# Kernel optimization log

Hardware: AMD Instinct MI355X
Metric: run time of the kernel (lower is better)

Reference implementation:

```python
import jax, jax.numpy as jnp
import numpy as np

IGNORE = 5
N_CLASS = 5
MAX_VIEWS = 2048
MAX_VIEWS_BG = 4096


def setup_inputs() -> dict:
    key = jax.random.key(0)
    ks = jax.random.split(key, 8)
    B, C, H, W = 8, 512, 128, 128
    HF, WF = 1024, 1024
    feats = jax.random.normal(ks[0], (B, C, H, W), dtype=jnp.float32)
    labels = jax.random.uniform(ks[1], (B, HF, WF, N_CLASS), dtype=jnp.float32)
    predicts = jax.random.randint(ks[2], (B, H, W), 0, N_CLASS).astype(jnp.int32)
    s = 0.02
    w1 = jax.random.normal(ks[3], (512, 512), jnp.float32) * s
    b1 = jnp.zeros((512,), jnp.float32)
    w2 = jax.random.normal(ks[4], (256, 512), jnp.float32) * s
    b2 = jnp.zeros((256,), jnp.float32)
    w3 = jax.random.normal(ks[5], (256, 256), jnp.float32) * s
    b3 = jnp.zeros((256,), jnp.float32)
    return dict(feats=feats, labels=labels, predicts=predicts,
                w1=w1, b1=b1, w2=w2, b2=b2, w3=w3, b3=b3)


def _leaky(x):
    return jnp.where(x >= 0, x, 0.2 * x)


def _proj_head(x, w1, b1, w2, b2, w3, b3):
    # Linear -> LeakyReLU(0.2) -> Linear -> LeakyReLU(0.2) -> Linear, then L2-normalize (dim=1)
    h = _leaky(x @ w1.T + b1)
    h = _leaky(h @ w2.T + b2)
    h = h @ w3.T + b3
    nrm = jnp.maximum(jnp.linalg.norm(h, axis=1, keepdims=True), 1e-12)
    return h / nrm


def _sample_class(y_hat, y, feats0, c, mv):
    """Stratified hard/easy pixel selection for class c, padded to static size mv.
    Deterministic take-first-k replaces torch.randperm for reproducibility."""
    N = y_hat.shape[0]
    hard = (y_hat == c) & (y != c)
    easy = (y_hat == c) & (y == c)
    nh = hard.sum().astype(jnp.int32)
    ne = easy.sum().astype(jnp.int32)
    cnt = nh + ne
    valid = (cnt > 1).astype(jnp.int32)   # classes with <=1 pixel are skipped in the original
    n_sel = jnp.minimum(cnt, mv) * valid
    both = (2 * nh >= n_sel) & (2 * ne >= n_sel)
    hk = jnp.where(both, n_sel // 2,
                   jnp.where(2 * nh >= n_sel, n_sel - ne, nh))
    ek = n_sel - hk
    idx = jnp.arange(N, dtype=jnp.int32)
    hsel = hard & ((jnp.cumsum(hard) - 1) < hk)   # first hk hard pixels
    esel = easy & ((jnp.cumsum(easy) - 1) < ek)   # first ek easy pixels
    # stream-compaction: hard first, then easy, then padding
    sort_key = jnp.where(hsel, idx, jnp.where(esel, idx + N, 2 * N))
    order = jnp.argsort(sort_key)[:mv]            # static slice of size mv
    row_ok = jnp.arange(mv) < n_sel
    X = feats0[order] * row_ok[:, None]           # zero-pad invalid rows
    yc = jnp.where(row_ok, c, IGNORE)
    return X, yc.astype(jnp.int32)


def reference(feats, labels, predicts, w1, b1, w2, b2, w3, b3):
    B, C, H, W = feats.shape
    lab = jnp.argmax(labels, axis=-1)             # [B, HF, WF]
    sh, sw = lab.shape[1] // H, lab.shape[2] // W
    lab_ds = lab[:, ::sh, ::sw]                   # nearest-neighbor downsample (integer factor)
    # original _hard_anchor_sampling returns inside the batch loop -> only image 0 contributes
    y_hat = lab_ds[0].reshape(-1).astype(jnp.int32)
    y = predicts[0].reshape(-1).astype(jnp.int32)
    feats0 = feats[0].transpose(1, 2, 0).reshape(H * W, C)  # NHWC flatten
    Xs, ys = [], []
    for c in range(N_CLASS):                      # static small class loop
        mv = MAX_VIEWS_BG if c == 0 else MAX_VIEWS
        Xc, yc = _sample_class(y_hat, y, feats0, c, mv)
        Xs.append(Xc)
        ys.append(yc)
    X_ = jnp.concatenate(Xs, axis=0)              # [MV_bg + 4*MV, 512]
    y_ = jnp.concatenate(ys, axis=0)
    anchors = _proj_head(X_, w1, b1, w2, b2, w3, b3)
    return anchors, y_
```

## Files before the change

kernel.cpp:

```cpp
#include <hip/hip_runtime.h>

#define HW 16384
#define IGN 5
#define ROWS_TOTAL 12288
#define ANCH_ELEMS (ROWS_TOTAL * 256)

typedef __bf16 bf16x8 __attribute__((ext_vector_type(8)));
typedef float f32x4 __attribute__((ext_vector_type(4)));
typedef unsigned long long ull;

#define GLDS16(g, l)                                                                     \
    __builtin_amdgcn_global_load_lds((__attribute__((address_space(1))) const void*)(g), \
                                     (__attribute__((address_space(3))) void*)(l), 16, 0, 0)

__device__ __forceinline__ int swz_off(int row, int chunk) {
    return row * 64 + ((chunk ^ (row & 7)) * 8);
}

__global__ void prep_fused(const float* __restrict__ labels, const int* __restrict__ predicts,
                           int* __restrict__ y_hat, ull* __restrict__ maskH,
                           ull* __restrict__ maskE, int* __restrict__ fwd,
                           const float* __restrict__ w1, const float* __restrict__ w2,
                           const float* __restrict__ w3, __bf16* __restrict__ w1b,
                           __bf16* __restrict__ w2b, __bf16* __restrict__ w3b,
                           const float* __restrict__ F, __bf16* __restrict__ Xb) {
    __shared__ float t[64][68];
    int bid = blockIdx.x;
    int tid = threadIdx.x;
    if (bid < 64) {
        int p = bid * 256 + tid;
        int pr = p >> 7, pc = p & 127;
        const float* lp = labels + ((size_t)(pr * 8) * 1024 + (size_t)(pc * 8)) * 5;
        float best = lp[0];
        int bi = 0;
#pragma unroll
        for (int c = 1; c < 5; ++c) {
            float v = lp[c];
            if (v > best) { best = v; bi = c; }
        }
        y_hat[p] = bi;
        if (p < ROWS_TOTAL) fwd[p] = -1;
        int yy = predicts[p];
        int chunk = p >> 6;
        int lane = tid & 63;
#pragma unroll
        for (int c = 0; c < 5; ++c) {
            ull mh = __ballot(bi == c && yy != c);
            ull me = __ballot(bi == c && yy == c);
            if (lane == 0) {
                maskH[c * 256 + chunk] = mh;
                maskE[c * 256 + chunk] = me;
            }
        }
    } else if (bid < 512) {
        int base = ((bid - 64) * 256 + tid) * 4;
        if (base < 262144) {
            float4 v = *(const float4*)(w1 + base);
            w1b[base + 0] = (__bf16)v.x; w1b[base + 1] = (__bf16)v.y;
            w1b[base + 2] = (__bf16)v.z; w1b[base + 3] = (__bf16)v.w;
        } else if (base < 393216) {
            int o = base - 262144;
            float4 v = *(const float4*)(w2 + o);
            w2b[o + 0] = (__bf16)v.x; w2b[o + 1] = (__bf16)v.y;
            w2b[o + 2] = (__bf16)v.z; w2b[o + 3] = (__bf16)v.w;
        } else {
            int o = base - 393216;
            float4 v = *(const float4*)(w3 + o);
            w3b[o + 0] = (__bf16)v.x; w3b[o + 1] = (__bf16)v.y;
            w3b[o + 2] = (__bf16)v.z; w3b[o + 3] = (__bf16)v.w;
        }
    } else {
        int cid = bid - 512;
        int pb = (cid & 255) * 64;
        int chb = (cid >> 8) * 64;
        int row = tid >> 2;
        int seg = tid & 3;
        const float* src = F + (size_t)(chb + row) * HW + pb + seg * 16;
#pragma unroll
        for (int k = 0; k < 4; ++k)
            *(float4*)&t[row][seg * 16 + k * 4] = *(const float4*)(src + k * 4);
        __syncthreads();
        int p = tid >> 2;
        __bf16* dst = Xb + (size_t)(pb + p) * 512 + chb + seg * 16;
        bf16x8 o0, o1;
#pragma unroll
        for (int j = 0; j < 8; ++j) o0[j] = (__bf16)t[seg * 16 + j][p];
#pragma unroll
        for (int j = 0; j < 8; ++j) o1[j] = (__bf16)t[seg * 16 + 8 + j][p];
        *(bf16x8*)dst = o0;
        *(bf16x8*)(dst + 8) = o1;
    }
}

__global__ void scan_kernel(const ull* __restrict__ maskH, const ull* __restrict__ maskE,
                            int* __restrict__ baseH, int* __restrict__ baseE,
                            int* __restrict__ nsel, int* __restrict__ hkA,
                            int* __restrict__ ekA) {
    int c = threadIdx.x >> 6;
    int lane = threadIdx.x & 63;
    if (c >= 5) return;
    int ph[4], pe[4];
    int sh = 0, se = 0;
#pragma unroll
    for (int k = 0; k < 4; ++k) {
        int ch = lane * 4 + k;
        ph[k] = sh;
        sh += __popcll(maskH[c * 256 + ch]);
        pe[k] = se;
        se += __popcll(maskE[c * 256 + ch]);
    }
    int incH = sh, incE = se;
#pragma unroll
    for (int d = 1; d < 64; d <<= 1) {
        int t = __shfl_up(incH, d);
        if (lane >= d) incH += t;
        t = __shfl_up(incE, d);
        if (lane >= d) incE += t;
    }
    int exH = incH - sh, exE = incE - se;
#pragma unroll
    for (int k = 0; k < 4; ++k) {
        baseH[c * 256 + lane * 4 + k] = exH + ph[k];
        baseE[c * 256 + lane * 4 + k] = exE + pe[k];
    }
    int nh = __shfl(incH, 63), ne = __shfl(incE, 63);
    if (lane == 0) {
        int mv = (c == 0) ? 4096 : 2048;
        int cnt = nh + ne;
        int n_sel = (cnt > 1) ? ((cnt < mv) ? cnt : mv) : 0;
        int hk;
        if ((2 * nh >= n_sel) && (2 * ne >= n_sel)) hk = n_sel >> 1;
        else if (2 * nh >= n_sel) hk = n_sel - ne;
        else hk = nh;
        nsel[c] = n_sel;
        hkA[c] = hk;
        ekA[c] = n_sel - hk;
    }
}

__global__ void write_inv_kernel(const int* __restrict__ y_hat,
                                 const ull* __restrict__ maskH, const ull* __restrict__ maskE,
                                 const int* __restrict__ baseH, const int* __restrict__ baseE,
                                 const int* __restrict__ hkA, const int* __restrict__ ekA,
                                 const int* __restrict__ nsel, int* __restrict__ fwd,
                                 float* __restrict__ out) {
    int p = blockIdx.x * 256 + threadIdx.x;
    int chunk = p >> 6;
    int lane = threadIdx.x & 63;
    int c = y_hat[p];
    ull mh = maskH[c * 256 + chunk];
    ull me = maskE[c * 256 + chunk];
    ull below = (1ull << lane) - 1ull;
    int cls_base = (c == 0) ? 0 : 4096 + (c - 1) * 2048;
    int res = -1;
    if ((mh >> lane) & 1ull) {
        int pos = baseH[c * 256 + chunk] + __popcll(mh & below);
        if (pos < hkA[c]) res = cls_base + pos;
    } else if ((me >> lane) & 1ull) {
        int pos = baseE[c * 256 + chunk] + __popcll(me & below);
        if (pos < ekA[c]) res = cls_base + hkA[c] + pos;
    }
    if (res >= 0) fwd[res] = p;
    if (p < ROWS_TOTAL) {
        int cc, rin;
        if (p < 4096) { cc = 0; rin = p; }
        else { cc = 1 + ((p - 4096) >> 11); rin = (p - 4096) & 2047; }
        out[ANCH_ELEMS + p] = (float)(rin < nsel[cc] ? cc : IGN);
    }
}

__global__ __launch_bounds__(256) void gemm_bt(const __bf16* __restrict__ A,
                                               const int* __restrict__ fwd,
                                               const __bf16* __restrict__ Bw,
                                               const float* __restrict__ bias,
                                               __bf16* __restrict__ C, int N, int K,
                                               int leaky) {
    const int BK = 64;
    __shared__ __bf16 As[64 * 64];
    __shared__ __bf16 Bs[128 * 64];
    int tid = threadIdx.x;
    int lane = tid & 63;
    int wave_base = tid & 0xC0;
    int wave = tid >> 6;
    int wm = (wave >> 1) * 32, wn = (wave & 1) * 64;
    int mb = blockIdx.x * 64, nb = blockIdx.y * 128;
    int l15 = lane & 15, quad = lane >> 4;

    const __bf16* srcA[2];
    const __bf16* srcB[4];
#pragma unroll
    for (int r = 0; r < 2; ++r) {
        int cc = tid + r * 256;
        int row = cc >> 3, ch = cc & 7;
        int g = mb + row;
        int pix = fwd ? fwd[g] : g;
        if (pix < 0) pix = 0;
        srcA[r] = A + (size_t)pix * K + ((ch ^ (row & 7)) * 8);
    }
#pragma unroll
    for (int r = 0; r < 4; ++r) {
        int cc = tid + r * 256;
        int row = cc >> 3, ch = cc & 7;
        srcB[r] = Bw + (size_t)(nb + row) * K + ((ch ^ (row & 7)) * 8);
    }

    f32x4 acc[2][4] = {};

    for (int kt = 0; kt < K; kt += BK) {
#pragma unroll
        for (int r = 0; r < 2; ++r)
            GLDS16(srcA[r] + kt, As + (size_t)(r * 256 + wave_base) * 8);
#pragma unroll
        for (int r = 0; r < 4; ++r)
            GLDS16(srcB[r] + kt, Bs + (size_t)(r * 256 + wave_base) * 8);
        __syncthreads();
#pragma unroll
        for (int kk = 0; kk < 2; ++kk) {
            bf16x8 af[2], bq[4];
#pragma unroll
            for (int i = 0; i < 2; ++i)
                af[i] = *(const bf16x8*)(As + swz_off(wm + i * 16 + l15, quad + kk * 4));
#pragma unroll
            for (int j = 0; j < 4; ++j)
                bq[j] = *(const bf16x8*)(Bs + swz_off(wn + j * 16 + l15, quad + kk * 4));
#pragma unroll
            for (int i = 0; i < 2; ++i)
#pragma unroll
                for (int j = 0; j < 4; ++j)
                    acc[i][j] = __builtin_amdgcn_mfma_f32_16x16x32_bf16(af[i], bq[j], acc[i][j], 0, 0, 0);
        }
        __syncthreads();
    }

#pragma unroll
    for (int i = 0; i < 2; ++i) {
#pragma unroll
        for (int j = 0; j < 4; ++j) {
            int col = nb + wn + j * 16 + l15;
            float bv = bias[col];
#pragma unroll
            for (int r = 0; r < 4; ++r) {
                int row = mb + wm + i * 16 + quad * 4 + r;
                float v = acc[i][j][r] + bv;
                if (leaky) v = (v >= 0.f) ? v : 0.2f * v;
                C[(size_t)row * N + col] = (__bf16)v;
            }
        }
    }
}

__global__ __launch_bounds__(256) void gemm23_norm(const __bf16* __restrict__ H1,
                                                   const __bf16* __restrict__ W2b,
                                                   const float* __restrict__ b2,
                                                   const __bf16* __restrict__ W3b,
                                                   const float* __restrict__ b3,
                                                   const int* __restrict__ fwd,
                                                   float* __restrict__ out) {
    __shared__ __bf16 As[32 * 64];
    __shared__ __bf16 Ws[256 * 64];
    __shared__ __bf16 H2s[4][32 * 64];
    __shared__ float nrm[32];
    int tid = threadIdx.x;
    int lane = tid & 63, wave = tid >> 6;
    int wave_base = tid & 0xC0;
    int l15 = lane & 15, quad = lane >> 4;
    int mb = blockIdx.x * 32;
    int wn = wave * 64;

    if (tid < 32) nrm[tid] = 0.f;

    int rowA = tid >> 3, chA = tid & 7;
    const __bf16* srcA = H1 + (size_t)(mb + rowA) * 512 + ((chA ^ (rowA & 7)) * 8);
    const __bf16* srcW2[8];
#pragma unroll
    for (int r = 0; r < 8; ++r) {
        int cc = tid + r * 256;
        int row = cc >> 3, ch = cc & 7;
        srcW2[r] = W2b + (size_t)row * 512 + ((ch ^ (row & 7)) * 8);
    }

    f32x4 acc[2][4] = {};
    for (int kt = 0; kt < 512; kt += 64) {
        GLDS16(srcA + kt, As + (size_t)wave_base * 8);
#pragma unroll
        for (int r = 0; r < 8; ++r)
            GLDS16(srcW2[r] + kt, Ws + (size_t)(r * 256 + wave_base) * 8);
        __syncthreads();
#pragma unroll
        for (int kk = 0; kk < 2; ++kk) {
            bf16x8 af[2], bq[4];
#pragma unroll
            for (int i = 0; i < 2; ++i)
                af[i] = *(const bf16x8*)(As + swz_off(i * 16 + l15, quad + kk * 4));
#pragma unroll
            for (int j = 0; j < 4; ++j)
                bq[j] = *(const bf16x8*)(Ws + swz_off(wn + j * 16 + l15, quad + kk * 4));
#pragma unroll
            for (int i = 0; i < 2; ++i)
#pragma unroll
                for (int j = 0; j < 4; ++j)
                    acc[i][j] = __builtin_amdgcn_mfma_f32_16x16x32_bf16(af[i], bq[j], acc[i][j], 0, 0, 0);
        }
        __syncthreads();
    }

#pragma unroll
    for (int i = 0; i < 2; ++i) {
#pragma unroll
        for (int j = 0; j < 4; ++j) {
            int col = wn + j * 16 + l15;
            float bv = b2[col];
            int ktb = col >> 6;
            int chunk = (col >> 3) & 7;
#pragma unroll
            for (int r = 0; r < 4; ++r) {
                int row = i * 16 + quad * 4 + r;
                float v = acc[i][j][r] + bv;
                v = (v >= 0.f) ? v : 0.2f * v;
                H2s[ktb][row * 64 + ((chunk ^ (row & 7)) * 8) + (col & 7)] = (__bf16)v;
            }
        }
    }
    __syncthreads();

    const __bf16* srcW3[8];
#pragma unroll
    for (int r = 0; r < 8; ++r) {
        int cc = tid + r * 256;
        int row = cc >> 3, ch = cc & 7;
        srcW3[r] = W3b + (size_t)row * 256 + ((ch ^ (row & 7)) * 8);
    }
    f32x4 acc3[2][4] = {};
    for (int ktb = 0; ktb < 4; ++ktb) {
#pragma unroll
        for (int r = 0; r < 8; ++r)
            GLDS16(srcW3[r] + ktb * 64, Ws + (size_t)(r * 256 + wave_base) * 8);
        __syncthreads();
#pragma unroll
        for (int kk = 0; kk < 2; ++kk) {
            bf16x8 af[2], bq[4];
#pragma unroll
            for (int i = 0; i < 2; ++i)
                af[i] = *(const bf16x8*)(&H2s[ktb][0] + swz_off(i * 16 + l15, quad + kk * 4));
#pragma unroll
            for (int j = 0; j < 4; ++j)
                bq[j] = *(const bf16x8*)(Ws + swz_off(wn + j * 16 + l15, quad + kk * 4));
#pragma unroll
            for (int i = 0; i < 2; ++i)
#pragma unroll
                for (int j = 0; j < 4; ++j)
                    acc3[i][j] = __builtin_amdgcn_mfma_f32_16x16x32_bf16(af[i], bq[j], acc3[i][j], 0, 0, 0);
        }
        __syncthreads();
    }

    float vs[2][4][4];
    float ss[2][4];
#pragma unroll
    for (int i = 0; i < 2; ++i)
#pragma unroll
        for (int r = 0; r < 4; ++r) ss[i][r] = 0.f;
#pragma unroll
    for (int i = 0; i < 2; ++i) {
#pragma unroll
        for (int j = 0; j < 4; ++j) {
            int col = wn + j * 16 + l15;
            float bv = b3[col];
#pragma unroll
            for (int r = 0; r < 4; ++r) {
                float v = acc3[i][j][r] + bv;
                vs[i][j][r] = v;
                ss[i][r] += v * v;
            }
        }
    }
#pragma unroll
    for (int i = 0; i < 2; ++i) {
#pragma unroll
        for (int r = 0; r < 4; ++r) {
            float s = ss[i][r];
            s += __shfl_xor(s, 1);
            s += __shfl_xor(s, 2);
            s += __shfl_xor(s, 4);
            s += __shfl_xor(s, 8);
            if (l15 == 0) atomicAdd(&nrm[i * 16 + quad * 4 + r], s);
        }
    }
    __syncthreads();
    if (tid < 32) {
        float f = 1.0f / fmaxf(sqrtf(nrm[tid]), 1e-12f);
        nrm[tid] = (fwd[mb + tid] >= 0) ? f : 0.f;
    }
    __syncthreads();
#pragma unroll
    for (int i = 0; i < 2; ++i) {
#pragma unroll
        for (int j = 0; j < 4; ++j) {
            int col = wn + j * 16 + l15;
#pragma unroll
            for (int r = 0; r < 4; ++r) {
                int row = i * 16 + quad * 4 + r;
                out[(size_t)(mb + row) * 256 + col] = vs[i][j][r] * nrm[row];
            }
        }
    }
}

extern "C" void kernel_launch(void* const* d_in, const int* in_sizes, int n_in,
                              void* d_out, int out_size, void* d_ws, size_t ws_size,
                              hipStream_t stream) {
    const float* feats = (const float*)d_in[0];
    const float* labels = (const float*)d_in[1];
    const int* predicts = (const int*)d_in[2];
    const float* w1 = (const float*)d_in[3];
    const float* b1 = (const float*)d_in[4];
    const float* w2 = (const float*)d_in[5];
    const float* b2 = (const float*)d_in[6];
    const float* w3 = (const float*)d_in[7];
    const float* b3 = (const float*)d_in[8];
    float* out = (float*)d_out;
    char* ws = (char*)d_ws;

    int* y_hat = (int*)(ws + 0);
    int* fwd = (int*)(ws + (64 << 10));
    int* nsel = (int*)(ws + (128 << 10));
    int* hkA = (int*)(ws + (128 << 10) + 64);
    int* ekA = (int*)(ws + (128 << 10) + 128);
    ull* maskH = (ull*)(ws + (136 << 10));
    ull* maskE = (ull*)(ws + (148 << 10));
    int* baseH = (int*)(ws + (160 << 10));
    int* baseE = (int*)(ws + (168 << 10));
    __bf16* w1b = (__bf16*)(ws + (256 << 10));
    __bf16* w2b = (__bf16*)(ws + (768 << 10));
    __bf16* w3b = (__bf16*)(ws + (1024 << 10));
    __bf16* Xb = (__bf16*)(ws + (2ull << 20));
    __bf16* H1 = (__bf16*)(ws + (18ull << 20));

    prep_fused<<<2560, 256, 0, stream>>>(labels, predicts, y_hat, maskH, maskE, fwd,
                                         w1, w2, w3, w1b, w2b, w3b, feats, Xb);
    scan_kernel<<<1, 320, 0, stream>>>(maskH, maskE, baseH, baseE, nsel, hkA, ekA);
    write_inv_kernel<<<64, 256, 0, stream>>>(y_hat, maskH, maskE, baseH, baseE, hkA, ekA,
                                             nsel, fwd, out);
    gemm_bt<<<dim3(192, 4), 256, 0, stream>>>(Xb, fwd, w1b, b1, H1, 512, 512, 1);
    gemm23_norm<<<384, 256, 0, stream>>>(H1, w2b, b2, w3b, b3, fwd, out);
}
```

Before: 412.5 us.

## Fuse scan and index compaction into GEMM kernels, prefetch first tiles early

Removes the separate scan and inverse-index kernels. Each GEMM1 block now recomputes the per-class prefix sums from the ballot masks and builds its own 64-row gather list in shared memory. GEMM23 recomputes n_sel to apply the validity mask and write the labels. The first weight tiles are issued before this index work so their loads overlap it, and W3 loading is hoisted ahead of the H2 epilogue. The cost is two fewer launches and a serialized pipeline, traded for redundant per-block scan work and a serial bit-walk loop in wave 0.

```diff
diff --git a/kernel.cpp b/kernel.cpp
--- a/kernel.cpp
+++ b/kernel.cpp
@@ -17,9 +17,13 @@
     return row * 64 + ((chunk ^ (row & 7)) * 8);
 }
 
+__device__ __forceinline__ void cls_of(int mb, int& cc, int& r0, int& mv) {
+    if (mb < 4096) { cc = 0; r0 = mb; mv = 4096; }
+    else { cc = 1 + ((mb - 4096) >> 11); r0 = (mb - 4096) & 2047; mv = 2048; }
+}
+
 __global__ void prep_fused(const float* __restrict__ labels, const int* __restrict__ predicts,
-                           int* __restrict__ y_hat, ull* __restrict__ maskH,
-                           ull* __restrict__ maskE, int* __restrict__ fwd,
+                           ull* __restrict__ maskH, ull* __restrict__ maskE,
                            const float* __restrict__ w1, const float* __restrict__ w2,
                            const float* __restrict__ w3, __bf16* __restrict__ w1b,
                            __bf16* __restrict__ w2b, __bf16* __restrict__ w3b,
@@ -38,8 +42,6 @@
             float v = lp[c];
             if (v > best) { best = v; bi = c; }
         }
-        y_hat[p] = bi;
-        if (p < ROWS_TOTAL) fwd[p] = -1;
         int yy = predicts[p];
         int chunk = p >> 6;
         int lane = tid & 63;
@@ -92,92 +94,16 @@
     }
 }
 
-__global__ void scan_kernel(const ull* __restrict__ maskH, const ull* __restrict__ maskE,
-                            int* __restrict__ baseH, int* __restrict__ baseE,
-                            int* __restrict__ nsel, int* __restrict__ hkA,
-                            int* __restrict__ ekA) {
-    int c = threadIdx.x >> 6;
-    int lane = threadIdx.x & 63;
-    if (c >= 5) return;
-    int ph[4], pe[4];
-    int sh = 0, se = 0;
-#pragma unroll
-    for (int k = 0; k < 4; ++k) {
-        int ch = lane * 4 + k;
-        ph[k] = sh;
-        sh += __popcll(maskH[c * 256 + ch]);
-        pe[k] = se;
-        se += __popcll(maskE[c * 256 + ch]);
-    }
-    int incH = sh, incE = se;
-#pragma unroll
-    for (int d = 1; d < 64; d <<= 1) {
-        int t = __shfl_up(incH, d);
-        if (lane >= d) incH += t;
-        t = __shfl_up(incE, d);
-        if (lane >= d) incE += t;
-    }
-    int exH = incH - sh, exE = incE - se;
-#pragma unroll
-    for (int k = 0; k < 4; ++k) {
-        baseH[c * 256 + lane * 4 + k] = exH + ph[k];
-        baseE[c * 256 + lane * 4 + k] = exE + pe[k];
-    }
-    int nh = __shfl(incH, 63), ne = __shfl(incE, 63);
-    if (lane == 0) {
-        int mv = (c == 0) ? 4096 : 2048;
-        int cnt = nh + ne;
-        int n_sel = (cnt > 1) ? ((cnt < mv) ? cnt : mv) : 0;
-        int hk;
-        if ((2 * nh >= n_sel) && (2 * ne >= n_sel)) hk = n_sel >> 1;
-        else if (2 * nh >= n_sel) hk = n_sel - ne;
-        else hk = nh;
-        nsel[c] = n_sel;
-        hkA[c] = hk;
-        ekA[c] = n_sel - hk;
-    }
-}
-
-__global__ void write_inv_kernel(const int* __restrict__ y_hat,
-                                 const ull* __restrict__ maskH, const ull* __restrict__ maskE,
-                                 const int* __restrict__ baseH, const int* __restrict__ baseE,
-                                 const int* __restrict__ hkA, const int* __restrict__ ekA,
-                                 const int* __restrict__ nsel, int* __restrict__ fwd,
-                                 float* __restrict__ out) {
-    int p = blockIdx.x * 256 + threadIdx.x;
-    int chunk = p >> 6;
-    int lane = threadIdx.x & 63;
-    int c = y_hat[p];
-    ull mh = maskH[c * 256 + chunk];
-    ull me = maskE[c * 256 + chunk];
-    ull below = (1ull << lane) - 1ull;
-    int cls_base = (c == 0) ? 0 : 4096 + (c - 1) * 2048;
-    int res = -1;
-    if ((mh >> lane) & 1ull) {
-        int pos = baseH[c * 256 + chunk] + __popcll(mh & below);
-        if (pos < hkA[c]) res = cls_base + pos;
-    } else if ((me >> lane) & 1ull) {
-        int pos = baseE[c * 256 + chunk] + __popcll(me & below);
-        if (pos < ekA[c]) res = cls_base + hkA[c] + pos;
-    }
-    if (res >= 0) fwd[res] = p;
-    if (p < ROWS_TOTAL) {
-        int cc, rin;
-        if (p < 4096) { cc = 0; rin = p; }
-        else { cc = 1 + ((p - 4096) >> 11); rin = (p - 4096) & 2047; }
-        out[ANCH_ELEMS + p] = (float)(rin < nsel[cc] ? cc : IGN);
-    }
-}
-
-__global__ __launch_bounds__(256) void gemm_bt(const __bf16* __restrict__ A,
-                                               const int* __restrict__ fwd,
-                                               const __bf16* __restrict__ Bw,
-                                               const float* __restrict__ bias,
-                                               __bf16* __restrict__ C, int N, int K,
-                                               int leaky) {
-    const int BK = 64;
+__global__ __launch_bounds__(256) void gemm1_bt(const __bf16* __restrict__ A,
+                                                const ull* __restrict__ maskH,
+                                                const ull* __restrict__ maskE,
+                                                const __bf16* __restrict__ Bw,
+                                                const float* __restrict__ bias,
+                                                __bf16* __restrict__ C) {
+    const int K = 512, N = 512, BK = 64;
     __shared__ __bf16 As[64 * 64];
     __shared__ __bf16 Bs[128 * 64];
+    __shared__ int fwd_s[64];
     int tid = threadIdx.x;
     int lane = tid & 63;
     int wave_base = tid & 0xC0;
@@ -186,23 +112,95 @@
     int mb = blockIdx.x * 64, nb = blockIdx.y * 128;
     int l15 = lane & 15, quad = lane >> 4;
 
+    const __bf16* srcB[4];
+#pragma unroll
+    for (int r = 0; r < 4; ++r) {
+        int cc2 = tid + r * 256;
+        int row = cc2 >> 3, ch = cc2 & 7;
+        srcB[r] = Bw + (size_t)(nb + row) * K + ((ch ^ (row & 7)) * 8);
+    }
+#pragma unroll
+    for (int r = 0; r < 4; ++r)
+        GLDS16(srcB[r], Bs + (size_t)(r * 256 + wave_base) * 8);
+
+    if (wave == 0) {
+        int cc, r0, mv;
+        cls_of(mb, cc, r0, mv);
+        const ull* MH = maskH + cc * 256;
+        const ull* ME = maskE + cc * 256;
+        ull mh[4], me[4];
+        int ph[4], pe[4];
+        int sh = 0, se = 0;
+#pragma unroll
+        for (int k = 0; k < 4; ++k) {
+            int ch = lane * 4 + k;
+            mh[k] = MH[ch];
+            me[k] = ME[ch];
+            ph[k] = sh; sh += __popcll(mh[k]);
+            pe[k] = se; se += __popcll(me[k]);
+        }
+        int incH = sh, incE = se;
+#pragma unroll
+        for (int d = 1; d < 64; d <<= 1) {
+            int tt = __shfl_up(incH, d);
+            if (lane >= d) incH += tt;
+            tt = __shfl_up(incE, d);
+            if (lane >= d) incE += tt;
+        }
+        int exH = incH - sh, exE = incE - se;
+        int nh = __shfl(incH, 63), ne = __shfl(incE, 63);
+        int cnt = nh + ne;
+        int n_sel = (cnt > 1) ? ((cnt < mv) ? cnt : mv) : 0;
+        int hk;
+        if ((2 * nh >= n_sel) && (2 * ne >= n_sel)) hk = n_sel >> 1;
+        else if (2 * nh >= n_sel) hk = n_sel - ne;
+        else hk = nh;
+        int ek = n_sel - hk;
+        fwd_s[lane] = -1;
+        int lo = r0, hi = min(r0 + 64, hk);
+#pragma unroll
+        for (int k = 0; k < 4; ++k) {
+            int base = exH + ph[k];
+            ull mm = mh[k];
+            if (base < hi && base + __popcll(mm) > lo) {
+                int j = 0;
+                while (mm) {
+                    int b = __ffsll(mm) - 1;
+                    mm &= mm - 1;
+                    int rk = base + j; ++j;
+                    if (rk >= lo && rk < hi) fwd_s[rk - r0] = (lane * 4 + k) * 64 + b;
+                }
+            }
+        }
+        int elo = r0 - hk;
+        if (elo < 0) elo = 0;
+        int ehi = min(r0 + 64 - hk, ek);
+#pragma unroll
+        for (int k = 0; k < 4; ++k) {
+            int base = exE + pe[k];
+            ull mm = me[k];
+            if (base < ehi && base + __popcll(mm) > elo) {
+                int j = 0;
+                while (mm) {
+                    int b = __ffsll(mm) - 1;
+                    mm &= mm - 1;
+                    int rk = base + j; ++j;
+                    if (rk >= elo && rk < ehi) fwd_s[hk + rk - r0] = (lane * 4 + k) * 64 + b;
+                }
+            }
+        }
+    }
+    __syncthreads();
+
     const __bf16* srcA[2];
-    const __bf16* srcB[4];
 #pragma unroll
     for (int r = 0; r < 2; ++r) {
-        int cc = tid + r * 256;
-        int row = cc >> 3, ch = cc & 7;
-        int g = mb + row;
-        int pix = fwd ? fwd[g] : g;
+        int cc2 = tid + r * 256;
+        int row = cc2 >> 3, ch = cc2 & 7;
+        int pix = fwd_s[row];
         if (pix < 0) pix = 0;
         srcA[r] = A + (size_t)pix * K + ((ch ^ (row & 7)) * 8);
     }
-#pragma unroll
-    for (int r = 0; r < 4; ++r) {
-        int cc = tid + r * 256;
-        int row = cc >> 3, ch = cc & 7;
-        srcB[r] = Bw + (size_t)(nb + row) * K + ((ch ^ (row & 7)) * 8);
-    }
 
     f32x4 acc[2][4] = {};
 
@@ -210,9 +208,11 @@
 #pragma unroll
         for (int r = 0; r < 2; ++r)
             GLDS16(srcA[r] + kt, As + (size_t)(r * 256 + wave_base) * 8);
-#pragma unroll
-        for (int r = 0; r < 4; ++r)
-            GLDS16(srcB[r] + kt, Bs + (size_t)(r * 256 + wave_base) * 8);
+        if (kt) {
+#pragma unroll
+            for (int r = 0; r < 4; ++r)
+                GLDS16(srcB[r] + kt, Bs + (size_t)(r * 256 + wave_base) * 8);
+        }
         __syncthreads();
 #pragma unroll
         for (int kk = 0; kk < 2; ++kk) {
@@ -242,7 +242,7 @@
             for (int r = 0; r < 4; ++r) {
                 int row = mb + wm + i * 16 + quad * 4 + r;
                 float v = acc[i][j][r] + bv;
-                if (leaky) v = (v >= 0.f) ? v : 0.2f * v;
+                v = (v >= 0.f) ? v : 0.2f * v;
                 C[(size_t)row * N + col] = (__bf16)v;
             }
         }
@@ -254,7 +254,8 @@
                                                    const float* __restrict__ b2,
                                                    const __bf16* __restrict__ W3b,
                                                    const float* __restrict__ b3,
-                                                   const int* __restrict__ fwd,
+                                                   const ull* __restrict__ maskH,
+                                                   const ull* __restrict__ maskE,
                                                    float* __restrict__ out) {
     __shared__ __bf16 As[32 * 64];
     __shared__ __bf16 Ws[256 * 64];
@@ -266,25 +267,49 @@
     int l15 = lane & 15, quad = lane >> 4;
     int mb = blockIdx.x * 32;
     int wn = wave * 64;
-
-    if (tid < 32) nrm[tid] = 0.f;
+    int cc, r0, mv;
+    cls_of(mb, cc, r0, mv);
 
     int rowA = tid >> 3, chA = tid & 7;
     const __bf16* srcA = H1 + (size_t)(mb + rowA) * 512 + ((chA ^ (rowA & 7)) * 8);
     const __bf16* srcW2[8];
 #pragma unroll
     for (int r = 0; r < 8; ++r) {
-        int cc = tid + r * 256;
-        int row = cc >> 3, ch = cc & 7;
+        int cc2 = tid + r * 256;
+        int row = cc2 >> 3, ch = cc2 & 7;
         srcW2[r] = W2b + (size_t)row * 512 + ((ch ^ (row & 7)) * 8);
     }
+    GLDS16(srcA, As + (size_t)wave_base * 8);
+#pragma unroll
+    for (int r = 0; r < 8; ++r)
+        GLDS16(srcW2[r], Ws + (size_t)(r * 256 + wave_base) * 8);
+
+    int n_sel = 0;
+    if (wave == 0) {
+        int sh = 0, se = 0;
+#pragma unroll
+        for (int k = 0; k < 4; ++k) {
+            sh += __popcll(maskH[cc * 256 + lane * 4 + k]);
+            se += __popcll(maskE[cc * 256 + lane * 4 + k]);
+        }
+#pragma unroll
+        for (int d = 1; d < 64; d <<= 1) {
+            sh += __shfl_xor(sh, d);
+            se += __shfl_xor(se, d);
+        }
+        int cnt = sh + se;
+        n_sel = (cnt > 1) ? ((cnt < mv) ? cnt : mv) : 0;
+    }
+    if (tid < 32) nrm[tid] = 0.f;
 
     f32x4 acc[2][4] = {};
     for (int kt = 0; kt < 512; kt += 64) {
-        GLDS16(srcA + kt, As + (size_t)wave_base * 8);
-#pragma unroll
-        for (int r = 0; r < 8; ++r)
-            GLDS16(srcW2[r] + kt, Ws + (size_t)(r * 256 + wave_base) * 8);
+        if (kt) {
+            GLDS16(srcA + kt, As + (size_t)wave_base * 8);
+#pragma unroll
+            for (int r = 0; r < 8; ++r)
+                GLDS16(srcW2[r] + kt, Ws + (size_t)(r * 256 + wave_base) * 8);
+        }
         __syncthreads();
 #pragma unroll
         for (int kk = 0; kk < 2; ++kk) {
@@ -303,6 +328,17 @@
         }
         __syncthreads();
     }
+
+    const __bf16* srcW3[8];
+#pragma unroll
+    for (int r = 0; r < 8; ++r) {
+        int cc2 = tid + r * 256;
+        int row = cc2 >> 3, ch = cc2 & 7;
+        srcW3[r] = W3b + (size_t)row * 256 + ((ch ^ (row & 7)) * 8);
+    }
+#pragma unroll
+    for (int r = 0; r < 8; ++r)
+        GLDS16(srcW3[r], Ws + (size_t)(r * 256 + wave_base) * 8);
 
 #pragma unroll
     for (int i = 0; i < 2; ++i) {
@@ -323,19 +359,14 @@
     }
     __syncthreads();
 
-    const __bf16* srcW3[8];
-#pragma unroll
-    for (int r = 0; r < 8; ++r) {
-        int cc = tid + r * 256;
-        int row = cc >> 3, ch = cc & 7;
-        srcW3[r] = W3b + (size_t)row * 256 + ((ch ^ (row & 7)) * 8);
-    }
     f32x4 acc3[2][4] = {};
     for (int ktb = 0; ktb < 4; ++ktb) {
-#pragma unroll
-        for (int r = 0; r < 8; ++r)
-            GLDS16(srcW3[r] + ktb * 64, Ws + (size_t)(r * 256 + wave_base) * 8);
-        __syncthreads();
+        if (ktb) {
+#pragma unroll
+            for (int r = 0; r < 8; ++r)
+                GLDS16(srcW3[r] + ktb * 64, Ws + (size_t)(r * 256 + wave_base) * 8);
+            __syncthreads();
+        }
 #pragma unroll
         for (int kk = 0; kk < 2; ++kk) {
             bf16x8 af[2], bq[4];
@@ -389,7 +420,9 @@
     __syncthreads();
     if (tid < 32) {
         float f = 1.0f / fmaxf(sqrtf(nrm[tid]), 1e-12f);
-        nrm[tid] = (fwd[mb + tid] >= 0) ? f : 0.f;
+        int ok = (r0 + tid) < n_sel;
+        nrm[tid] = ok ? f : 0.f;
+        out[ANCH_ELEMS + mb + tid] = (float)(ok ? cc : IGN);
     }
     __syncthreads();
 #pragma unroll
@@ -421,26 +454,16 @@
     float* out = (float*)d_out;
     char* ws = (char*)d_ws;
 
-    int* y_hat = (int*)(ws + 0);
-    int* fwd = (int*)(ws + (64 << 10));
-    int* nsel = (int*)(ws + (128 << 10));
-    int* hkA = (int*)(ws + (128 << 10) + 64);
-    int* ekA = (int*)(ws + (128 << 10) + 128);
     ull* maskH = (ull*)(ws + (136 << 10));
     ull* maskE = (ull*)(ws + (148 << 10));
-    int* baseH = (int*)(ws + (160 << 10));
-    int* baseE = (int*)(ws + (168 << 10));
     __bf16* w1b = (__bf16*)(ws + (256 << 10));
     __bf16* w2b = (__bf16*)(ws + (768 << 10));
     __bf16* w3b = (__bf16*)(ws + (1024 << 10));
     __bf16* Xb = (__bf16*)(ws + (2ull << 20));
     __bf16* H1 = (__bf16*)(ws + (18ull << 20));
 
-    prep_fused<<<2560, 256, 0, stream>>>(labels, predicts, y_hat, maskH, maskE, fwd,
+    prep_fused<<<2560, 256, 0, stream>>>(labels, predicts, maskH, maskE,
                                          w1, w2, w3, w1b, w2b, w3b, feats, Xb);
-    scan_kernel<<<1, 320, 0, stream>>>(maskH, maskE, baseH, baseE, nsel, hkA, ekA);
-    write_inv_kernel<<<64, 256, 0, stream>>>(y_hat, maskH, maskE, baseH, baseE, hkA, ekA,
-                                             nsel, fwd, out);
-    gemm_bt<<<dim3(192, 4), 256, 0, stream>>>(Xb, fwd, w1b, b1, H1, 512, 512, 1);
-    gemm23_norm<<<384, 256, 0, stream>>>(H1, w2b, b2, w3b, b3, fwd, out);
-}
+    gemm1_bt<<<dim3(192, 4), 256, 0, stream>>>(Xb, maskH, maskE, w1b, b1, H1);
+    gemm23_norm<<<384, 256, 0, stream>>>(H1, w2b, b2, w3b, b3, maskH, maskE, out);
+}
```

Measured after the change: 410.4 us (median of 2 runs). Within noise of the previous version (-0.5%).
